# Performance work log

Hardware: AMD Instinct MI355X
Metric: run time of the kernel (lower is better)

## Reference

```python
import jax, jax.numpy as jnp
import numpy as np

K = 9          # kernel_size
PAD = K // 2   # 'same' padding, stride 1
SIGMA = 1.0
EPS = 1e-5     # BatchNorm eps

def _windows(a):
    # a: (B, C, L) -> (B, C, K, L); zero-padded sliding windows (== F.unfold semantics)
    L = a.shape[-1]
    ap = jnp.pad(a, ((0, 0), (0, 0), (PAD, PAD)))
    return jnp.stack([ap[:, :, k:k + L] for k in range(K)], axis=2)

def setup_inputs() -> dict:
    key = jax.random.key(0)
    ks = jax.random.split(key, 4)
    B, Cin, Cout, L = 8, 256, 256, 16384
    x = jax.random.normal(ks[0], (B, Cin, L), jnp.float32)
    coords = jax.random.uniform(ks[1], (B, 3, L), jnp.float32)
    conv_w = jax.random.normal(ks[2], (Cout, Cin, K), jnp.float32) * np.float32(1.0 / np.sqrt(Cin * K))
    conv_b = jnp.zeros((Cout,), jnp.float32)
    gamma = jnp.ones((Cout,), jnp.float32)
    beta = jnp.zeros((Cout,), jnp.float32)
    return {"x": x, "coords": coords, "conv_w": conv_w, "conv_b": conv_b, "gamma": gamma, "beta": beta}

def reference(x, coords, conv_w, conv_b, gamma, beta):
    # --- WeightedConv1D: Gaussian coordinate weights on each unfolded window element ---
    cw = _windows(coords)                                      # (B, 3, K, L)
    d2 = jnp.sum((cw - coords[:, :, None, :]) ** 2, axis=1)    # (B, K, L) squared dist to window center
    w = jnp.exp(-d2 / (2.0 * SIGMA ** 2))                      # (B, K, L) Gaussian weights
    xw = _windows(x) * w[:, None, :, :]                        # (B, Cin, K, L) weighted windows
    y = jnp.einsum('bckl,ock->bol', xw, conv_w) + conv_b[None, :, None]  # (B, Cout, L)
    # --- BatchNorm1d (training-mode batch statistics, biased variance) + ReLU ---
    mu = jnp.mean(y, axis=(0, 2), keepdims=True)
    var = jnp.var(y, axis=(0, 2), keepdims=True)
    yhat = (y - mu) * jax.lax.rsqrt(var + EPS)
    out = jax.nn.relu(yhat * gamma[None, :, None] + beta[None, :, None])
    # Dropout with drop=0.0 is the identity.
    return out
```

## Files before the change

kernel.cpp:

```cpp
#include <hip/hip_runtime.h>
#include <hip/hip_bf16.h>


typedef float        f32x4  __attribute__((ext_vector_type(4)));
typedef float        f32x16 __attribute__((ext_vector_type(16)));
typedef short        bf16x8 __attribute__((ext_vector_type(8)));
typedef unsigned int u32x4  __attribute__((ext_vector_type(4)));

#define LLEN 16384

__device__ __forceinline__ unsigned short bf16bits(float a) {
  return __builtin_bit_cast(unsigned short, __float2bfloat16(a));
}
__device__ __forceinline__ unsigned cvt_pk_bf16(float lo, float hi) {
  unsigned r;
  asm("v_cvt_pk_bf16_f32 %0, %1, %2" : "=v"(r) : "v"(lo), "v"(hi));
  return r;
}
__device__ __forceinline__ void gload16(const void* g, void* l) {
  __builtin_amdgcn_global_load_lds(
      (const __attribute__((address_space(1))) unsigned int*)g,
      (__attribute__((address_space(3))) unsigned int*)l, 16, 0, 0);
}

__global__ void k_prep(const float* __restrict__ cw,
                       unsigned short* __restrict__ A_r4,
                       unsigned short* __restrict__ A_gl,
                       float* __restrict__ sums, int big) {
  const int idx = blockIdx.x * 256 + threadIdx.x;
  if (idx < 1024) sums[idx] = 0.0f;
  const int o   = idx / 2304;
  const int rem = idx - o * 2304;
  const int c   = rem / 9;
  const int kk  = rem - c * 9;
  const unsigned short bits = bf16bits(cw[idx]);
  A_r4[((size_t)kk * 256 + o) * 256 + c] = bits;
  if (big) {
    const int cc = c >> 6, c6 = c & 63;
    const int u = (c6 >> 3) ^ (o & 7);
    A_gl[(size_t)((kk * 4 + cc) << 14) + ((o * 8 + u) << 3) + (c6 & 7)] = bits;
  }
}

__global__ void k_w(const float* __restrict__ coords, float* __restrict__ wbuf) {
  const int gidx = blockIdx.x * 256 + threadIdx.x;
  const int b = gidx >> 14, l = gidx & (LLEN - 1);
  const float* cb = coords + (size_t)b * 3 * LLEN;
  const float c0 = cb[l], c1 = cb[LLEN + l], c2v = cb[2 * LLEN + l];
#pragma unroll
  for (int kk = 0; kk < 9; ++kk) {
    const int lc = l + kk - 4;
    float a0 = 0.f, a1 = 0.f, a2 = 0.f;
    if (lc >= 0 && lc < LLEN) { a0 = cb[lc]; a1 = cb[LLEN + lc]; a2 = cb[2 * LLEN + lc]; }
    const float d0 = a0 - c0, d1 = a1 - c1, d2 = a2 - c2v;
    wbuf[(((size_t)(b * 9 + kk)) << 14) + l] = __expf(-0.5f * (d0 * d0 + d1 * d1 + d2 * d2));
  }
}

__global__ void k_xT(const float* __restrict__ x, unsigned short* __restrict__ xT) {
  __shared__ unsigned short T[64][72];
  const int tid = threadIdx.x, bid = blockIdx.x;
  const int ct = bid & 3, lt = (bid >> 2) & 255, b = bid >> 10;
  const int l0 = lt << 6, c0 = ct << 6;
#pragma unroll
  for (int p = 0; p < 4; ++p) {
    const int cl = p * 16 + (tid >> 4), ll = (tid & 15) << 2;
    const f32x4 v = *reinterpret_cast<const f32x4*>(
        x + (((size_t)(b * 256 + c0 + cl)) << 14) + l0 + ll);
#pragma unroll
    for (int q = 0; q < 4; ++q) T[cl][ll + q] = bf16bits(v[q]);
  }
  __syncthreads();
#pragma unroll
  for (int pass = 0; pass < 2; ++pass) {
    const int n = tid + pass * 256;
    const int ll = n >> 3, u = n & 7;
    const int l = l0 + ll;
    const int gsl = (u ^ (l & 7)) << 3;
    u32x4 val;
#pragma unroll
    for (int q = 0; q < 4; ++q)
      val[q] = (unsigned)T[gsl + 2 * q][ll] | ((unsigned)T[gsl + 2 * q + 1][ll] << 16);
    *reinterpret_cast<u32x4*>(xT + (((size_t)((b << 14) + l)) << 8) + (ct << 6) + (u << 3)) = val;
  }
}

__global__ __launch_bounds__(512, 2) void k_gemm_dma(
    const unsigned short* __restrict__ xT, const float* __restrict__ wbuf,
    const unsigned short* __restrict__ Agl, const float* __restrict__ convb,
    const unsigned short* __restrict__ zeros, float* __restrict__ y,
    float* __restrict__ sums) {
  __shared__ __align__(16) unsigned short Ash[2][16384];
  __shared__ __align__(16) unsigned short Xsh[2][17408];

  const int tid = threadIdx.x, lane = tid & 63, wv = tid >> 6;
  const int wm = wv >> 2, wn = wv & 3;
  const int l31 = lane & 31, hi5 = lane >> 5;
  const int b = blockIdx.x >> 6, lt = blockIdx.x & 63, l0 = lt << 8;

  f32x16 acc[4][2];
#pragma unroll
  for (int i = 0; i < 4; ++i)
#pragma unroll
    for (int j = 0; j < 2; ++j) acc[i][j] = (f32x16)(0.0f);

  auto dmaA = [&](int ab, int kk, int cc) {
#pragma unroll
    for (int call = 0; call < 4; ++call) {
      const int n0 = ((call << 3) + wv) << 6;
      gload16(Agl + (((size_t)((kk << 2) + cc)) << 14) + (((size_t)(n0 + lane)) << 3),
              (char*)&Ash[ab][0] + n0 * 16);
    }
  };
  auto dmaX = [&](int xb, int ncc, int slot) {
    const int id = (slot << 3) + wv;
    if (id < 34) {
      const int n0 = id << 6;
      const int n = n0 + lane;
      const int r = n >> 3, u = n & 7;
      const int lp = l0 - 4 + r;
      const unsigned short* src =
          (lp >= 0 && lp < LLEN)
              ? xT + (((size_t)((b << 14) + lp)) << 8) + (ncc << 6) + (u << 3)
              : zeros;
      gload16(src, (char*)&Xsh[xb][0] + n0 * 16);
    }
  };

  dmaA(0, 0, 0);
#pragma unroll
  for (int s = 0; s < 5; ++s) dmaX(0, 0, s);
  float wl[2], wt[2];
#pragma unroll
  for (int nt = 0; nt < 2; ++nt)
    wl[nt] = wbuf[((size_t)(b * 9) << 14) + l0 + wn * 64 + nt * 32 + l31];
  __syncthreads();

  int ab = 0;
#pragma unroll 1
  for (int cc = 0; cc < 4; ++cc) {
    const int xb = cc & 1;
    const char* XshB = (const char*)&Xsh[xb][0];
#pragma unroll 1
    for (int kk = 0; kk < 9; ++kk) {
      const bool last = (cc == 3) && (kk == 8);
      const int nkk = (kk == 8) ? 0 : kk + 1;
      const int ncc = (kk == 8) ? cc + 1 : cc;
      if (!last) {
        dmaA(ab ^ 1, nkk, ncc);
#pragma unroll
        for (int nt = 0; nt < 2; ++nt)
          wt[nt] = wbuf[((size_t)(b * 9 + nkk) << 14) + l0 + wn * 64 + nt * 32 + l31];
      }
      if (cc < 3 && kk < 5) dmaX(xb ^ 1, cc + 1, kk);

      const char* AshB = (const char*)&Ash[ab][0];
#pragma unroll
      for (int ks = 0; ks < 4; ++ks) {
        const int g = (ks << 1) + hi5;
        bf16x8 bfr[2];
#pragma unroll
        for (int nt = 0; nt < 2; ++nt) {
          const int rr = wn * 64 + nt * 32 + l31 + kk;
          const u32x4 xv = *reinterpret_cast<const u32x4*>(
              XshB + rr * 128 + ((g ^ ((rr + 4) & 7)) << 4));
          u32x4 o4;
#pragma unroll
          for (int q = 0; q < 4; ++q) {
            const float flo = __builtin_bit_cast(float, xv[q] << 16) * wl[nt];
            const float fhi = __builtin_bit_cast(float, xv[q] & 0xffff0000u) * wl[nt];
            o4[q] = cvt_pk_bf16(flo, fhi);
          }
          bfr[nt] = __builtin_bit_cast(bf16x8, o4);
        }
#pragma unroll
        for (int mt = 0; mt < 4; ++mt) {
          const int o = wm * 128 + mt * 32 + l31;
          const bf16x8 af = *reinterpret_cast<const bf16x8*>(
              AshB + o * 128 + ((g ^ (l31 & 7)) << 4));
#pragma unroll
          for (int nt = 0; nt < 2; ++nt)
            acc[mt][nt] = __builtin_amdgcn_mfma_f32_32x32x16_bf16(af, bfr[nt],
                                                                  acc[mt][nt], 0, 0, 0);
        }
      }
      __syncthreads();
      ab ^= 1;
      wl[0] = wt[0]; wl[1] = wt[1];
    }
  }

  float* red = reinterpret_cast<float*>(&Xsh[0][0]);
  red[tid] = 0.0f;
  __syncthreads();
#pragma unroll
  for (int mt = 0; mt < 4; ++mt) {
#pragma unroll
    for (int v = 0; v < 16; ++v) {
      const int o = wm * 128 + mt * 32 + (v & 3) + 8 * (v >> 2) + 4 * hi5;
      const float cb = convb[o];
      float s = 0.f, s2 = 0.f;
#pragma unroll
      for (int nt = 0; nt < 2; ++nt) {
        const int l = l0 + wn * 64 + nt * 32 + l31;
        const float yv = acc[mt][nt][v] + cb;
        y[(((size_t)b * 256 + o) << 14) + l] = yv;
        s += yv; s2 += yv * yv;
      }
#pragma unroll
      for (int d = 1; d < 32; d <<= 1) { s += __shfl_xor(s, d); s2 += __shfl_xor(s2, d); }
      if (l31 == 0) { atomicAdd(&red[o], s); atomicAdd(&red[o + 256], s2); }
    }
  }
  __syncthreads();
  atomicAdd(&sums[tid], red[tid]);
}

__global__ __launch_bounds__(512, 2) void k_gemm_fb(
    const float* __restrict__ x, const float* __restrict__ wbuf,
    const unsigned short* __restrict__ Aperm, const float* __restrict__ convb,
    float* __restrict__ y, float* __restrict__ sums) {
  __shared__ __align__(16) unsigned short Ash[2][256 * 64];
  __shared__ __align__(16) unsigned short Xsh[2][264 * 72];

  const int tid  = threadIdx.x;
  const int lane = tid & 63, wv = tid >> 6;
  const int wm = wv >> 2, wn = wv & 3;
  const int hi = lane >> 4, lo16 = lane & 15;
  const int b  = blockIdx.x >> 6, lt = blockIdx.x & 63;
  const int l0 = lt << 8;
  const int nbase = wn * 64 + lo16;
  const int c = tid >> 3, rg = tid & 7;

  f32x4 acc[8][4];
#pragma unroll
  for (int i = 0; i < 8; ++i)
#pragma unroll
    for (int j = 0; j < 4; ++j) acc[i][j] = f32x4{0.f, 0.f, 0.f, 0.f};

  auto loadA = [&](int kk, int cc, u32x4 (&dst)[4]) {
#pragma unroll
    for (int p = 0; p < 4; ++p) {
      const int row = p * 64 + (tid >> 3);
      dst[p] = *reinterpret_cast<const u32x4*>(
          Aperm + ((size_t)kk * 256 + row) * 256 + cc * 64 + ((tid & 7) << 3));
    }
  };
  auto writeA = [&](int ab, const u32x4 (&src)[4]) {
#pragma unroll
    for (int p = 0; p < 4; ++p) {
      const int row  = p * 64 + (tid >> 3);
      const unsigned byte = (unsigned)(row * 128 + (((tid & 7) ^ (row & 7)) << 4));
      *reinterpret_cast<u32x4*>(reinterpret_cast<char*>(&Ash[ab][0]) + byte) = src[p];
    }
  };
  auto loadPiece = [&](int ncc, int i) -> f32x4 {
    const float* xrow = x + ((size_t)(b * 256 + ncc * 64 + c)) * LLEN;
    const int grp = rg + 8 * i;
    const int lx = l0 - 4 + grp * 4;
    f32x4 v = {0.f, 0.f, 0.f, 0.f};
    if (grp < 66 && lx >= 0 && lx <= LLEN - 4)
      v = *reinterpret_cast<const f32x4*>(xrow + lx);
    return v;
  };
  auto writePiece = [&](int xb, int i, const f32x4& v) {
    const int grp = rg + 8 * i;
    if (grp < 66) {
      unsigned short* base = &Xsh[xb][0] + (grp * 4) * 72 + c;
      base[0]   = bf16bits(v[0]);
      base[72]  = bf16bits(v[1]);
      base[144] = bf16bits(v[2]);
      base[216] = bf16bits(v[3]);
    }
  };

  {
    u32x4 a0[4];
    loadA(0, 0, a0);
    writeA(0, a0);
#pragma unroll
    for (int i = 0; i < 9; ++i) writePiece(0, i, loadPiece(0, i));
  }
  float wl[4];
#pragma unroll
  for (int nt = 0; nt < 4; ++nt)
    wl[nt] = wbuf[((size_t)(b * 9) << 14) + l0 + nbase + nt * 16];
  __syncthreads();

  int ab = 0;
  f32x4 xhold = {0.f, 0.f, 0.f, 0.f};

#pragma unroll 1
  for (int cc = 0; cc < 4; ++cc) {
    const int xb = cc & 1;
#pragma unroll 1
    for (int kk = 0; kk < 9; ++kk) {
      const int nkk = (kk == 8) ? 0 : kk + 1;
      const int ncc = (kk == 8) ? cc + 1 : cc;
      const bool has_next = (ncc < 4);

      u32x4 areg[4];
      if (has_next) loadA(nkk, ncc, areg);
      float wln[4] = {0.f, 0.f, 0.f, 0.f};
      if (has_next) {
#pragma unroll
        for (int nt = 0; nt < 4; ++nt)
          wln[nt] = wbuf[((size_t)(b * 9 + nkk) << 14) + l0 + nbase + nt * 16];
      }
      f32x4 xnew = {0.f, 0.f, 0.f, 0.f};
      if (cc < 3) xnew = loadPiece(cc + 1, kk);

      const char* AshB = reinterpret_cast<const char*>(&Ash[ab][0]);
      const char* XshB = reinterpret_cast<const char*>(&Xsh[xb][0]);
#pragma unroll
      for (int kb = 0; kb < 2; ++kb) {
        bf16x8 bfr[4];
#pragma unroll
        for (int nt = 0; nt < 4; ++nt) {
          const int r = nbase + nt * 16 + kk;
          const u32x4 xv = *reinterpret_cast<const u32x4*>(XshB + r * 144 + kb * 64 + hi * 16);
          const float wv2 = wl[nt];
          u32x4 o4;
#pragma unroll
          for (int q = 0; q < 4; ++q) {
            const float flo = __builtin_bit_cast(float, xv[q] << 16) * wv2;
            const float fhi = __builtin_bit_cast(float, xv[q] & 0xffff0000u) * wv2;
            o4[q] = cvt_pk_bf16(flo, fhi);
          }
          bfr[nt] = __builtin_bit_cast(bf16x8, o4);
        }
#pragma unroll
        for (int mt = 0; mt < 8; ++mt) {
          const int orow = wm * 128 + mt * 16 + lo16;
          const unsigned aoff = (unsigned)(orow * 128 + (((kb * 4 + hi) ^ (orow & 7)) << 4));
          const bf16x8 af = *reinterpret_cast<const bf16x8*>(AshB + aoff);
#pragma unroll
          for (int nt = 0; nt < 4; ++nt)
            acc[mt][nt] = __builtin_amdgcn_mfma_f32_16x16x32_bf16(af, bfr[nt],
                                                                  acc[mt][nt], 0, 0, 0);
        }
      }

      if (cc < 3 && kk >= 1) writePiece(xb ^ 1, kk - 1, xhold);
      if (cc < 3 && kk == 8) writePiece(xb ^ 1, 8, xnew);
      if (has_next) writeA(ab ^ 1, areg);

      __syncthreads();
      ab ^= 1;
      xhold = xnew;
#pragma unroll
      for (int nt = 0; nt < 4; ++nt) wl[nt] = wln[nt];
    }
  }

  float* red = reinterpret_cast<float*>(&Ash[0][0]);
  red[tid] = 0.0f;
  __syncthreads();
#pragma unroll
  for (int mt = 0; mt < 8; ++mt) {
#pragma unroll
    for (int v = 0; v < 4; ++v) {
      const int o = wm * 128 + mt * 16 + hi * 4 + v;
      const float cb = convb[o];
      float s = 0.f, s2 = 0.f;
#pragma unroll
      for (int nt = 0; nt < 4; ++nt) {
        const int l = l0 + nbase + nt * 16;
        const float yv = acc[mt][nt][v] + cb;
        y[(((size_t)b * 256 + o) << 14) + l] = yv;
        s += yv; s2 += yv * yv;
      }
#pragma unroll
      for (int d = 1; d < 16; d <<= 1) { s += __shfl_xor(s, d); s2 += __shfl_xor(s2, d); }
      if (lo16 == 0) { atomicAdd(&red[o], s); atomicAdd(&red[o + 256], s2); }
    }
  }
  __syncthreads();
  atomicAdd(&sums[tid], red[tid]);
}

__global__ void k_norm(float* __restrict__ y, const float* __restrict__ sums,
                       const float* __restrict__ gamma, const float* __restrict__ beta) {
  const size_t i0 = ((size_t)blockIdx.x * 256 + threadIdx.x) * 8;
  const int o = (int)((i0 >> 14) & 255);
  const float n = 131072.f;
  const float mu = sums[o] / n;
  float var = sums[256 + o] / n - mu * mu;
  var = fmaxf(var, 0.f);
  const float sc = rsqrtf(var + 1e-5f) * gamma[o];
  const float bb = beta[o] - mu * sc;
  f32x4 v0 = *reinterpret_cast<const f32x4*>(y + i0);
  f32x4 v1 = *reinterpret_cast<const f32x4*>(y + i0 + 4);
#pragma unroll
  for (int i = 0; i < 4; ++i) {
    v0[i] = fmaxf(v0[i] * sc + bb, 0.f);
    v1[i] = fmaxf(v1[i] * sc + bb, 0.f);
  }
  *reinterpret_cast<f32x4*>(y + i0) = v0;
  *reinterpret_cast<f32x4*>(y + i0 + 4) = v1;
}

extern "C" void kernel_launch(void* const* d_in, const int* in_sizes, int n_in,
                              void* d_out, int out_size, void* d_ws, size_t ws_size,
                              hipStream_t stream) {
  const float* x      = (const float*)d_in[0];
  const float* coords = (const float*)d_in[1];
  const float* conv_w = (const float*)d_in[2];
  const float* conv_b = (const float*)d_in[3];
  const float* gamma  = (const float*)d_in[4];
  const float* beta   = (const float*)d_in[5];
  float* out = (float*)d_out;

  float* sums = (float*)d_ws;
  const unsigned short* zeros = (const unsigned short*)((char*)d_ws + 2048);
  float* wbuf = (float*)((char*)d_ws + 4096);
  unsigned short* A_r4 = (unsigned short*)((char*)d_ws + 4096 + (size_t)8 * 9 * LLEN * 4);
  unsigned short* A_gl = A_r4 + 589824;
  unsigned short* xT   = A_gl + 589824;
  const size_t need = 4096 + (size_t)8 * 9 * LLEN * 4 + 2 * 1179648ull + 67108864ull;
  const int big = (ws_size >= need) ? 1 : 0;

  k_prep<<<2304, 256, 0, stream>>>(conv_w, A_r4, A_gl, sums, big);
  k_w<<<512, 256, 0, stream>>>(coords, wbuf);
  if (big) {
    k_xT<<<8192, 256, 0, stream>>>(x, xT);
    k_gemm_dma<<<512, 512, 0, stream>>>(xT, wbuf, A_gl, conv_b, zeros, out, sums);
  } else {
    k_gemm_fb<<<512, 512, 0, stream>>>(x, wbuf, A_r4, conv_b, out, sums);
  }
  k_norm<<<16384, 256, 0, stream>>>(out, sums, gamma, beta);
}
```

Baseline: 287.5 us.

## Pre-weight X tiles once in LDS per tap and store intermediate y as bf16

The GEMM kernel now loads x rows into registers, multiplies them by the Gaussian weight once per tap and stores weighted bf16 tiles into double-buffered LDS. This replaces the per-MFMA-fragment reweighting and the direct global-to-LDS DMA of X. A-fragment loads are grouped ahead of the MFMAs and wrapped in s_setprio. When enough workspace is available, the pre-norm y is written as bf16 rather than fp32, which halves that intermediate write and the norm kernel's read but adds rounding error before BatchNorm.

```diff
diff --git a/kernel.cpp b/kernel.cpp
--- a/kernel.cpp
+++ b/kernel.cpp
@@ -21,6 +21,12 @@
   __builtin_amdgcn_global_load_lds(
       (const __attribute__((address_space(1))) unsigned int*)g,
       (__attribute__((address_space(3))) unsigned int*)l, 16, 0, 0);
+}
+__device__ __forceinline__ float bflo(unsigned u) {
+  return __builtin_bit_cast(float, u << 16);
+}
+__device__ __forceinline__ float bfhi(unsigned u) {
+  return __builtin_bit_cast(float, u & 0xffff0000u);
 }
 
 __global__ void k_prep(const float* __restrict__ cw,
@@ -85,18 +91,20 @@
   }
 }
 
-__global__ __launch_bounds__(512, 2) void k_gemm_dma(
+template <int YBF>
+__global__ __launch_bounds__(512, 2) void k_gemm_w(
     const unsigned short* __restrict__ xT, const float* __restrict__ wbuf,
     const unsigned short* __restrict__ Agl, const float* __restrict__ convb,
-    const unsigned short* __restrict__ zeros, float* __restrict__ y,
+    float* __restrict__ yf, unsigned short* __restrict__ ybf,
     float* __restrict__ sums) {
   __shared__ __align__(16) unsigned short Ash[2][16384];
-  __shared__ __align__(16) unsigned short Xsh[2][17408];
+  __shared__ __align__(16) unsigned short Xw[2][264 * 64];
 
   const int tid = threadIdx.x, lane = tid & 63, wv = tid >> 6;
   const int wm = wv >> 2, wn = wv & 3;
   const int l31 = lane & 31, hi5 = lane >> 5;
   const int b = blockIdx.x >> 6, lt = blockIdx.x & 63, l0 = lt << 8;
+  const int rbase = tid >> 3, uu = tid & 7;
 
   f32x16 acc[4][2];
 #pragma unroll
@@ -112,85 +120,97 @@
               (char*)&Ash[ab][0] + n0 * 16);
     }
   };
-  auto dmaX = [&](int xb, int ncc, int slot) {
-    const int id = (slot << 3) + wv;
-    if (id < 34) {
-      const int n0 = id << 6;
-      const int n = n0 + lane;
-      const int r = n >> 3, u = n & 7;
-      const int lp = l0 - 4 + r;
-      const unsigned short* src =
-          (lp >= 0 && lp < LLEN)
-              ? xT + (((size_t)((b << 14) + lp)) << 8) + (ncc << 6) + (u << 3)
-              : zeros;
-      gload16(src, (char*)&Xsh[xb][0] + n0 * 16);
-    }
-  };
-
+  auto loadX = [&](int cc, int i) -> u32x4 {
+    u32x4 v = {0u, 0u, 0u, 0u};
+    if (i < 4 || tid < 64) {
+      const int r = rbase + 64 * i;
+      const int l = l0 - 4 + r;
+      if (l >= 0 && l < LLEN)
+        v = *reinterpret_cast<const u32x4*>(
+            xT + (((size_t)((b << 14) + l)) << 8) + cc * 64 + uu * 8);
+    }
+    return v;
+  };
+  auto stage = [&](int xwb, int nkk, const u32x4 (&xr)[5]) {
+    const float* wrow = wbuf + ((size_t)(b * 9 + nkk) << 14);
+#pragma unroll
+    for (int i = 0; i < 5; ++i) {
+      if (i < 4 || tid < 64) {
+        const int r = rbase + 64 * i;
+        int lo_ = l0 + r - nkk;
+        lo_ = lo_ < 0 ? 0 : (lo_ > LLEN - 1 ? LLEN - 1 : lo_);
+        const float wv2 = wrow[lo_];
+        u32x4 o4;
+#pragma unroll
+        for (int q = 0; q < 4; ++q)
+          o4[q] = cvt_pk_bf16(bflo(xr[i][q]) * wv2, bfhi(xr[i][q]) * wv2);
+        *reinterpret_cast<u32x4*>(
+            reinterpret_cast<char*>(&Xw[xwb][0]) + r * 128 + ((uu ^ 4) << 4)) = o4;
+      }
+    }
+  };
+
+  u32x4 xcur[5], xnext[5];
+#pragma unroll
+  for (int i = 0; i < 5; ++i) xcur[i] = loadX(0, i);
   dmaA(0, 0, 0);
-#pragma unroll
-  for (int s = 0; s < 5; ++s) dmaX(0, 0, s);
-  float wl[2], wt[2];
-#pragma unroll
-  for (int nt = 0; nt < 2; ++nt)
-    wl[nt] = wbuf[((size_t)(b * 9) << 14) + l0 + wn * 64 + nt * 32 + l31];
-  __syncthreads();
-
-  int ab = 0;
+  stage(0, 0, xcur);
+  __syncthreads();
+
+  int ab = 0, xwb = 0;
 #pragma unroll 1
   for (int cc = 0; cc < 4; ++cc) {
-    const int xb = cc & 1;
-    const char* XshB = (const char*)&Xsh[xb][0];
 #pragma unroll 1
     for (int kk = 0; kk < 9; ++kk) {
       const bool last = (cc == 3) && (kk == 8);
       const int nkk = (kk == 8) ? 0 : kk + 1;
       const int ncc = (kk == 8) ? cc + 1 : cc;
-      if (!last) {
-        dmaA(ab ^ 1, nkk, ncc);
-#pragma unroll
-        for (int nt = 0; nt < 2; ++nt)
-          wt[nt] = wbuf[((size_t)(b * 9 + nkk) << 14) + l0 + wn * 64 + nt * 32 + l31];
-      }
-      if (cc < 3 && kk < 5) dmaX(xb ^ 1, cc + 1, kk);
+      if (!last) dmaA(ab ^ 1, nkk, ncc);
+      if (cc < 3 && kk >= 4) xnext[kk - 4] = loadX(cc + 1, kk - 4);
 
       const char* AshB = (const char*)&Ash[ab][0];
+      const char* XwB  = (const char*)&Xw[xwb][0];
 #pragma unroll
       for (int ks = 0; ks < 4; ++ks) {
         const int g = (ks << 1) + hi5;
         bf16x8 bfr[2];
 #pragma unroll
         for (int nt = 0; nt < 2; ++nt) {
-          const int rr = wn * 64 + nt * 32 + l31 + kk;
-          const u32x4 xv = *reinterpret_cast<const u32x4*>(
-              XshB + rr * 128 + ((g ^ ((rr + 4) & 7)) << 4));
-          u32x4 o4;
-#pragma unroll
-          for (int q = 0; q < 4; ++q) {
-            const float flo = __builtin_bit_cast(float, xv[q] << 16) * wl[nt];
-            const float fhi = __builtin_bit_cast(float, xv[q] & 0xffff0000u) * wl[nt];
-            o4[q] = cvt_pk_bf16(flo, fhi);
-          }
-          bfr[nt] = __builtin_bit_cast(bf16x8, o4);
+          const int R = wn * 64 + nt * 32 + l31 + kk;
+          bfr[nt] = *reinterpret_cast<const bf16x8*>(
+              XwB + R * 128 + ((g ^ (R & 7)) << 4));
         }
+        bf16x8 afr[4];
 #pragma unroll
         for (int mt = 0; mt < 4; ++mt) {
           const int o = wm * 128 + mt * 32 + l31;
-          const bf16x8 af = *reinterpret_cast<const bf16x8*>(
+          afr[mt] = *reinterpret_cast<const bf16x8*>(
               AshB + o * 128 + ((g ^ (l31 & 7)) << 4));
+        }
+        __builtin_amdgcn_s_setprio(1);
+#pragma unroll
+        for (int mt = 0; mt < 4; ++mt)
 #pragma unroll
           for (int nt = 0; nt < 2; ++nt)
-            acc[mt][nt] = __builtin_amdgcn_mfma_f32_32x32x16_bf16(af, bfr[nt],
+            acc[mt][nt] = __builtin_amdgcn_mfma_f32_32x32x16_bf16(afr[mt], bfr[nt],
                                                                   acc[mt][nt], 0, 0, 0);
-        }
+        __builtin_amdgcn_s_setprio(0);
+      }
+
+      if (!last) {
+        if (kk < 8) stage(xwb ^ 1, nkk, xcur);
+        else        stage(xwb ^ 1, 0, xnext);
       }
       __syncthreads();
-      ab ^= 1;
-      wl[0] = wt[0]; wl[1] = wt[1];
-    }
-  }
-
-  float* red = reinterpret_cast<float*>(&Xsh[0][0]);
+      ab ^= 1; xwb ^= 1;
+    }
+    if (cc < 3) {
+#pragma unroll
+      for (int i = 0; i < 5; ++i) xcur[i] = xnext[i];
+    }
+  }
+
+  float* red = reinterpret_cast<float*>(&Xw[0][0]);
   red[tid] = 0.0f;
   __syncthreads();
 #pragma unroll
@@ -204,7 +224,9 @@
       for (int nt = 0; nt < 2; ++nt) {
         const int l = l0 + wn * 64 + nt * 32 + l31;
         const float yv = acc[mt][nt][v] + cb;
-        y[(((size_t)b * 256 + o) << 14) + l] = yv;
+        const size_t idx = (((size_t)b * 256 + o) << 14) + l;
+        if (YBF) ybf[idx] = bf16bits(yv);
+        else     yf[idx] = yv;
         s += yv; s2 += yv * yv;
       }
 #pragma unroll
@@ -322,11 +344,8 @@
           const float wv2 = wl[nt];
           u32x4 o4;
 #pragma unroll
-          for (int q = 0; q < 4; ++q) {
-            const float flo = __builtin_bit_cast(float, xv[q] << 16) * wv2;
-            const float fhi = __builtin_bit_cast(float, xv[q] & 0xffff0000u) * wv2;
-            o4[q] = cvt_pk_bf16(flo, fhi);
-          }
+          for (int q = 0; q < 4; ++q)
+            o4[q] = cvt_pk_bf16(bflo(xv[q]) * wv2, bfhi(xv[q]) * wv2);
           bfr[nt] = __builtin_bit_cast(bf16x8, o4);
         }
 #pragma unroll
@@ -379,7 +398,9 @@
   atomicAdd(&sums[tid], red[tid]);
 }
 
-__global__ void k_norm(float* __restrict__ y, const float* __restrict__ sums,
+template <int YBF>
+__global__ void k_norm(const float* __restrict__ yf, const unsigned short* __restrict__ ybf,
+                       float* __restrict__ out, const float* __restrict__ sums,
                        const float* __restrict__ gamma, const float* __restrict__ beta) {
   const size_t i0 = ((size_t)blockIdx.x * 256 + threadIdx.x) * 8;
   const int o = (int)((i0 >> 14) & 255);
@@ -389,15 +410,27 @@
   var = fmaxf(var, 0.f);
   const float sc = rsqrtf(var + 1e-5f) * gamma[o];
   const float bb = beta[o] - mu * sc;
-  f32x4 v0 = *reinterpret_cast<const f32x4*>(y + i0);
-  f32x4 v1 = *reinterpret_cast<const f32x4*>(y + i0 + 4);
+  f32x4 v0, v1;
+  if (YBF) {
+    const u32x4 u = *reinterpret_cast<const u32x4*>(ybf + i0);
+#pragma unroll
+    for (int i = 0; i < 4; ++i) {
+      const unsigned w = u[i];
+      float a = bflo(w), c = bfhi(w);
+      if (i < 2) { v0[2 * i] = a; v0[2 * i + 1] = c; }
+      else       { v1[2 * (i - 2)] = a; v1[2 * (i - 2) + 1] = c; }
+    }
+  } else {
+    v0 = *reinterpret_cast<const f32x4*>(yf + i0);
+    v1 = *reinterpret_cast<const f32x4*>(yf + i0 + 4);
+  }
 #pragma unroll
   for (int i = 0; i < 4; ++i) {
     v0[i] = fmaxf(v0[i] * sc + bb, 0.f);
     v1[i] = fmaxf(v1[i] * sc + bb, 0.f);
   }
-  *reinterpret_cast<f32x4*>(y + i0) = v0;
-  *reinterpret_cast<f32x4*>(y + i0 + 4) = v1;
+  *reinterpret_cast<f32x4*>(out + i0) = v0;
+  *reinterpret_cast<f32x4*>(out + i0 + 4) = v1;
 }
 
 extern "C" void kernel_launch(void* const* d_in, const int* in_sizes, int n_in,
@@ -412,21 +445,29 @@
   float* out = (float*)d_out;
 
   float* sums = (float*)d_ws;
-  const unsigned short* zeros = (const unsigned short*)((char*)d_ws + 2048);
   float* wbuf = (float*)((char*)d_ws + 4096);
   unsigned short* A_r4 = (unsigned short*)((char*)d_ws + 4096 + (size_t)8 * 9 * LLEN * 4);
   unsigned short* A_gl = A_r4 + 589824;
   unsigned short* xT   = A_gl + 589824;
-  const size_t need = 4096 + (size_t)8 * 9 * LLEN * 4 + 2 * 1179648ull + 67108864ull;
-  const int big = (ws_size >= need) ? 1 : 0;
+  unsigned short* ybf  = xT + 33554432;
+  const size_t need_big = 4096 + (size_t)8 * 9 * LLEN * 4 + 2 * 1179648ull + 67108864ull;
+  const size_t need_ybf = need_big + 67108864ull;
+  const int big  = (ws_size >= need_big) ? 1 : 0;
+  const int ybfp = (ws_size >= need_ybf) ? 1 : 0;
 
   k_prep<<<2304, 256, 0, stream>>>(conv_w, A_r4, A_gl, sums, big);
   k_w<<<512, 256, 0, stream>>>(coords, wbuf);
   if (big) {
     k_xT<<<8192, 256, 0, stream>>>(x, xT);
-    k_gemm_dma<<<512, 512, 0, stream>>>(xT, wbuf, A_gl, conv_b, zeros, out, sums);
+    if (ybfp) {
+      k_gemm_w<1><<<512, 512, 0, stream>>>(xT, wbuf, A_gl, conv_b, out, ybf, sums);
+      k_norm<1><<<16384, 256, 0, stream>>>(out, ybf, out, sums, gamma, beta);
+    } else {
+      k_gemm_w<0><<<512, 512, 0, stream>>>(xT, wbuf, A_gl, conv_b, out, ybf, sums);
+      k_norm<0><<<16384, 256, 0, stream>>>(out, ybf, out, sums, gamma, beta);
+    }
   } else {
     k_gemm_fb<<<512, 512, 0, stream>>>(x, wbuf, A_r4, conv_b, out, sums);
-  }
-  k_norm<<<16384, 256, 0, stream>>>(out, sums, gamma, beta);
-}
+    k_norm<0><<<16384, 256, 0, stream>>>(out, nullptr, out, sums, gamma, beta);
+  }
+}
```

Result: slower. 316.8 us (+10.2%).

## Switch GEMM to 16x16 MFMA tiles and stage pre-norm output in bf16

Applied to the files above, without the earlier changes.

Rewrites the main GEMM kernel to use 16x16x32 bf16 MFMA with an 8x4 accumulator tile per wave. It also issues LDS reads for the next k-half before the current MFMAs, to overlap loads with compute. When workspace allows, the pre-BatchNorm output is stored as bf16 in a scratch buffer instead of fp32 into the output. This halves that intermediate write and the norm kernel's read, and trims duplicate weight-layout writes in prep. The cost is extra rounding of y before normalization, and a different register footprint.

```diff
diff --git a/kernel.cpp b/kernel.cpp
--- a/kernel.cpp
+++ b/kernel.cpp
@@ -3,7 +3,6 @@
 
 
 typedef float        f32x4  __attribute__((ext_vector_type(4)));
-typedef float        f32x16 __attribute__((ext_vector_type(16)));
 typedef short        bf16x8 __attribute__((ext_vector_type(8)));
 typedef unsigned int u32x4  __attribute__((ext_vector_type(4)));
 
@@ -22,10 +21,15 @@
       (const __attribute__((address_space(1))) unsigned int*)g,
       (__attribute__((address_space(3))) unsigned int*)l, 16, 0, 0);
 }
+__device__ __forceinline__ float bflo(unsigned u) {
+  return __builtin_bit_cast(float, u << 16);
+}
+__device__ __forceinline__ float bfhi(unsigned u) {
+  return __builtin_bit_cast(float, u & 0xffff0000u);
+}
 
 __global__ void k_prep(const float* __restrict__ cw,
-                       unsigned short* __restrict__ A_r4,
-                       unsigned short* __restrict__ A_gl,
+                       unsigned short* __restrict__ AU,
                        float* __restrict__ sums, int big) {
   const int idx = blockIdx.x * 256 + threadIdx.x;
   if (idx < 1024) sums[idx] = 0.0f;
@@ -34,11 +38,12 @@
   const int c   = rem / 9;
   const int kk  = rem - c * 9;
   const unsigned short bits = bf16bits(cw[idx]);
-  A_r4[((size_t)kk * 256 + o) * 256 + c] = bits;
   if (big) {
     const int cc = c >> 6, c6 = c & 63;
     const int u = (c6 >> 3) ^ (o & 7);
-    A_gl[(size_t)((kk * 4 + cc) << 14) + ((o * 8 + u) << 3) + (c6 & 7)] = bits;
+    AU[(size_t)((kk * 4 + cc) << 14) + ((o * 8 + u) << 3) + (c6 & 7)] = bits;
+  } else {
+    AU[((size_t)kk * 256 + o) * 256 + c] = bits;
   }
 }
 
@@ -85,24 +90,26 @@
   }
 }
 
-__global__ __launch_bounds__(512, 2) void k_gemm_dma(
+template <int YBF>
+__global__ __launch_bounds__(512, 2) void k_gemm16(
     const unsigned short* __restrict__ xT, const float* __restrict__ wbuf,
     const unsigned short* __restrict__ Agl, const float* __restrict__ convb,
-    const unsigned short* __restrict__ zeros, float* __restrict__ y,
-    float* __restrict__ sums) {
+    const unsigned short* __restrict__ zeros, float* __restrict__ yf,
+    unsigned short* __restrict__ ybf, float* __restrict__ sums) {
   __shared__ __align__(16) unsigned short Ash[2][16384];
   __shared__ __align__(16) unsigned short Xsh[2][17408];
 
   const int tid = threadIdx.x, lane = tid & 63, wv = tid >> 6;
   const int wm = wv >> 2, wn = wv & 3;
-  const int l31 = lane & 31, hi5 = lane >> 5;
+  const int hi = lane >> 4, lo16 = lane & 15;
   const int b = blockIdx.x >> 6, lt = blockIdx.x & 63, l0 = lt << 8;
-
-  f32x16 acc[4][2];
-#pragma unroll
-  for (int i = 0; i < 4; ++i)
-#pragma unroll
-    for (int j = 0; j < 2; ++j) acc[i][j] = (f32x16)(0.0f);
+  const int nbase = wn * 64 + lo16;
+
+  f32x4 acc[8][4];
+#pragma unroll
+  for (int i = 0; i < 8; ++i)
+#pragma unroll
+    for (int j = 0; j < 4; ++j) acc[i][j] = f32x4{0.f, 0.f, 0.f, 0.f};
 
   auto dmaA = [&](int ab, int kk, int cc) {
 #pragma unroll
@@ -130,10 +137,10 @@
   dmaA(0, 0, 0);
 #pragma unroll
   for (int s = 0; s < 5; ++s) dmaX(0, 0, s);
-  float wl[2], wt[2];
-#pragma unroll
-  for (int nt = 0; nt < 2; ++nt)
-    wl[nt] = wbuf[((size_t)(b * 9) << 14) + l0 + wn * 64 + nt * 32 + l31];
+  float wl[4], wt[4];
+#pragma unroll
+  for (int nt = 0; nt < 4; ++nt)
+    wl[nt] = wbuf[((size_t)(b * 9) << 14) + l0 + nbase + nt * 16];
   __syncthreads();
 
   int ab = 0;
@@ -149,44 +156,75 @@
       if (!last) {
         dmaA(ab ^ 1, nkk, ncc);
 #pragma unroll
-        for (int nt = 0; nt < 2; ++nt)
-          wt[nt] = wbuf[((size_t)(b * 9 + nkk) << 14) + l0 + wn * 64 + nt * 32 + l31];
+        for (int nt = 0; nt < 4; ++nt)
+          wt[nt] = wbuf[((size_t)(b * 9 + nkk) << 14) + l0 + nbase + nt * 16];
       }
       if (cc < 3 && kk < 5) dmaX(xb ^ 1, cc + 1, kk);
 
       const char* AshB = (const char*)&Ash[ab][0];
-#pragma unroll
-      for (int ks = 0; ks < 4; ++ks) {
-        const int g = (ks << 1) + hi5;
-        bf16x8 bfr[2];
-#pragma unroll
-        for (int nt = 0; nt < 2; ++nt) {
-          const int rr = wn * 64 + nt * 32 + l31 + kk;
-          const u32x4 xv = *reinterpret_cast<const u32x4*>(
-              XshB + rr * 128 + ((g ^ ((rr + 4) & 7)) << 4));
-          u32x4 o4;
-#pragma unroll
-          for (int q = 0; q < 4; ++q) {
-            const float flo = __builtin_bit_cast(float, xv[q] << 16) * wl[nt];
-            const float fhi = __builtin_bit_cast(float, xv[q] & 0xffff0000u) * wl[nt];
-            o4[q] = cvt_pk_bf16(flo, fhi);
-          }
-          bfr[nt] = __builtin_bit_cast(bf16x8, o4);
-        }
-#pragma unroll
-        for (int mt = 0; mt < 4; ++mt) {
-          const int o = wm * 128 + mt * 32 + l31;
-          const bf16x8 af = *reinterpret_cast<const bf16x8*>(
-              AshB + o * 128 + ((g ^ (l31 & 7)) << 4));
-#pragma unroll
-          for (int nt = 0; nt < 2; ++nt)
-            acc[mt][nt] = __builtin_amdgcn_mfma_f32_32x32x16_bf16(af, bfr[nt],
-                                                                  acc[mt][nt], 0, 0, 0);
-        }
-      }
+      u32x4 xv0[4];
+#pragma unroll
+      for (int nt = 0; nt < 4; ++nt) {
+        const int rr = nbase + nt * 16 + kk;
+        xv0[nt] = *reinterpret_cast<const u32x4*>(
+            XshB + rr * 128 + ((hi ^ ((rr + 4) & 7)) << 4));
+      }
+      bf16x8 a0[8];
+#pragma unroll
+      for (int mt = 0; mt < 8; ++mt) {
+        const int o = wm * 128 + mt * 16 + lo16;
+        a0[mt] = *reinterpret_cast<const bf16x8*>(
+            AshB + o * 128 + ((hi ^ (lo16 & 7)) << 4));
+      }
+      bf16x8 b0[4];
+#pragma unroll
+      for (int nt = 0; nt < 4; ++nt) {
+        u32x4 o4;
+#pragma unroll
+        for (int q = 0; q < 4; ++q)
+          o4[q] = cvt_pk_bf16(bflo(xv0[nt][q]) * wl[nt], bfhi(xv0[nt][q]) * wl[nt]);
+        b0[nt] = __builtin_bit_cast(bf16x8, o4);
+      }
+      u32x4 xv1[4];
+#pragma unroll
+      for (int nt = 0; nt < 4; ++nt) {
+        const int rr = nbase + nt * 16 + kk;
+        xv1[nt] = *reinterpret_cast<const u32x4*>(
+            XshB + rr * 128 + (((4 + hi) ^ ((rr + 4) & 7)) << 4));
+      }
+#pragma unroll
+      for (int mt = 0; mt < 8; ++mt)
+#pragma unroll
+        for (int nt = 0; nt < 4; ++nt)
+          acc[mt][nt] = __builtin_amdgcn_mfma_f32_16x16x32_bf16(a0[mt], b0[nt],
+                                                                acc[mt][nt], 0, 0, 0);
+      bf16x8 a1[8];
+#pragma unroll
+      for (int mt = 0; mt < 8; ++mt) {
+        const int o = wm * 128 + mt * 16 + lo16;
+        a1[mt] = *reinterpret_cast<const bf16x8*>(
+            AshB + o * 128 + (((4 + hi) ^ (lo16 & 7)) << 4));
+      }
+      bf16x8 b1[4];
+#pragma unroll
+      for (int nt = 0; nt < 4; ++nt) {
+        u32x4 o4;
+#pragma unroll
+        for (int q = 0; q < 4; ++q)
+          o4[q] = cvt_pk_bf16(bflo(xv1[nt][q]) * wl[nt], bfhi(xv1[nt][q]) * wl[nt]);
+        b1[nt] = __builtin_bit_cast(bf16x8, o4);
+      }
+#pragma unroll
+      for (int mt = 0; mt < 8; ++mt)
+#pragma unroll
+        for (int nt = 0; nt < 4; ++nt)
+          acc[mt][nt] = __builtin_amdgcn_mfma_f32_16x16x32_bf16(a1[mt], b1[nt],
+                                                                acc[mt][nt], 0, 0, 0);
+
       __syncthreads();
       ab ^= 1;
-      wl[0] = wt[0]; wl[1] = wt[1];
+#pragma unroll
+      for (int nt = 0; nt < 4; ++nt) wl[nt] = wt[nt];
     }
   }
 
@@ -194,22 +232,24 @@
   red[tid] = 0.0f;
   __syncthreads();
 #pragma unroll
-  for (int mt = 0; mt < 4; ++mt) {
-#pragma unroll
-    for (int v = 0; v < 16; ++v) {
-      const int o = wm * 128 + mt * 32 + (v & 3) + 8 * (v >> 2) + 4 * hi5;
+  for (int mt = 0; mt < 8; ++mt) {
+#pragma unroll
+    for (int v = 0; v < 4; ++v) {
+      const int o = wm * 128 + mt * 16 + hi * 4 + v;
       const float cb = convb[o];
       float s = 0.f, s2 = 0.f;
 #pragma unroll
-      for (int nt = 0; nt < 2; ++nt) {
-        const int l = l0 + wn * 64 + nt * 32 + l31;
+      for (int nt = 0; nt < 4; ++nt) {
+        const int l = l0 + nbase + nt * 16;
         const float yv = acc[mt][nt][v] + cb;
-        y[(((size_t)b * 256 + o) << 14) + l] = yv;
+        const size_t idx = (((size_t)b * 256 + o) << 14) + l;
+        if (YBF) ybf[idx] = bf16bits(yv);
+        else     yf[idx] = yv;
         s += yv; s2 += yv * yv;
       }
 #pragma unroll
-      for (int d = 1; d < 32; d <<= 1) { s += __shfl_xor(s, d); s2 += __shfl_xor(s2, d); }
-      if (l31 == 0) { atomicAdd(&red[o], s); atomicAdd(&red[o + 256], s2); }
+      for (int d = 1; d < 16; d <<= 1) { s += __shfl_xor(s, d); s2 += __shfl_xor(s2, d); }
+      if (lo16 == 0) { atomicAdd(&red[o], s); atomicAdd(&red[o + 256], s2); }
     }
   }
   __syncthreads();
@@ -319,14 +359,10 @@
         for (int nt = 0; nt < 4; ++nt) {
           const int r = nbase + nt * 16 + kk;
           const u32x4 xv = *reinterpret_cast<const u32x4*>(XshB + r * 144 + kb * 64 + hi * 16);
-          const float wv2 = wl[nt];
           u32x4 o4;
 #pragma unroll
-          for (int q = 0; q < 4; ++q) {
-            const float flo = __builtin_bit_cast(float, xv[q] << 16) * wv2;
-            const float fhi = __builtin_bit_cast(float, xv[q] & 0xffff0000u) * wv2;
-            o4[q] = cvt_pk_bf16(flo, fhi);
-          }
+          for (int q = 0; q < 4; ++q)
+            o4[q] = cvt_pk_bf16(bflo(xv[q]) * wl[nt], bfhi(xv[q]) * wl[nt]);
           bfr[nt] = __builtin_bit_cast(bf16x8, o4);
         }
 #pragma unroll
@@ -379,7 +415,9 @@
   atomicAdd(&sums[tid], red[tid]);
 }
 
-__global__ void k_norm(float* __restrict__ y, const float* __restrict__ sums,
+template <int YBF>
+__global__ void k_norm(const float* __restrict__ yf, const unsigned short* __restrict__ ybf,
+                       float* __restrict__ out, const float* __restrict__ sums,
                        const float* __restrict__ gamma, const float* __restrict__ beta) {
   const size_t i0 = ((size_t)blockIdx.x * 256 + threadIdx.x) * 8;
   const int o = (int)((i0 >> 14) & 255);
@@ -389,15 +427,27 @@
   var = fmaxf(var, 0.f);
   const float sc = rsqrtf(var + 1e-5f) * gamma[o];
   const float bb = beta[o] - mu * sc;
-  f32x4 v0 = *reinterpret_cast<const f32x4*>(y + i0);
-  f32x4 v1 = *reinterpret_cast<const f32x4*>(y + i0 + 4);
+  f32x4 v0, v1;
+  if (YBF) {
+    const u32x4 u = *reinterpret_cast<const u32x4*>(ybf + i0);
+#pragma unroll
+    for (int i = 0; i < 4; ++i) {
+      const unsigned w = u[i];
+      float a = bflo(w), c = bfhi(w);
+      if (i < 2) { v0[2 * i] = a; v0[2 * i + 1] = c; }
+      else       { v1[2 * (i - 2)] = a; v1[2 * (i - 2) + 1] = c; }
+    }
+  } else {
+    v0 = *reinterpret_cast<const f32x4*>(yf + i0);
+    v1 = *reinterpret_cast<const f32x4*>(yf + i0 + 4);
+  }
 #pragma unroll
   for (int i = 0; i < 4; ++i) {
     v0[i] = fmaxf(v0[i] * sc + bb, 0.f);
     v1[i] = fmaxf(v1[i] * sc + bb, 0.f);
   }
-  *reinterpret_cast<f32x4*>(y + i0) = v0;
-  *reinterpret_cast<f32x4*>(y + i0 + 4) = v1;
+  *reinterpret_cast<f32x4*>(out + i0) = v0;
+  *reinterpret_cast<f32x4*>(out + i0 + 4) = v1;
 }
 
 extern "C" void kernel_launch(void* const* d_in, const int* in_sizes, int n_in,
@@ -414,19 +464,27 @@
   float* sums = (float*)d_ws;
   const unsigned short* zeros = (const unsigned short*)((char*)d_ws + 2048);
   float* wbuf = (float*)((char*)d_ws + 4096);
-  unsigned short* A_r4 = (unsigned short*)((char*)d_ws + 4096 + (size_t)8 * 9 * LLEN * 4);
-  unsigned short* A_gl = A_r4 + 589824;
-  unsigned short* xT   = A_gl + 589824;
-  const size_t need = 4096 + (size_t)8 * 9 * LLEN * 4 + 2 * 1179648ull + 67108864ull;
-  const int big = (ws_size >= need) ? 1 : 0;
-
-  k_prep<<<2304, 256, 0, stream>>>(conv_w, A_r4, A_gl, sums, big);
+  unsigned short* AU  = (unsigned short*)((char*)d_ws + 4096 + (size_t)8 * 9 * LLEN * 4);
+  unsigned short* xT  = AU + 589824;
+  unsigned short* ybf = xT + 33554432;
+  const size_t need_big = 4096 + (size_t)8 * 9 * LLEN * 4 + 1179648ull + 67108864ull;
+  const size_t need_ybf = need_big + 67108864ull;
+  const int big  = (ws_size >= need_big) ? 1 : 0;
+  const int ybfp = (ws_size >= need_ybf) ? 1 : 0;
+
+  k_prep<<<2304, 256, 0, stream>>>(conv_w, AU, sums, big);
   k_w<<<512, 256, 0, stream>>>(coords, wbuf);
   if (big) {
     k_xT<<<8192, 256, 0, stream>>>(x, xT);
-    k_gemm_dma<<<512, 512, 0, stream>>>(xT, wbuf, A_gl, conv_b, zeros, out, sums);
+    if (ybfp) {
+      k_gemm16<1><<<512, 512, 0, stream>>>(xT, wbuf, AU, conv_b, zeros, out, ybf, sums);
+      k_norm<1><<<16384, 256, 0, stream>>>(out, ybf, out, sums, gamma, beta);
+    } else {
+      k_gemm16<0><<<512, 512, 0, stream>>>(xT, wbuf, AU, conv_b, zeros, out, ybf, sums);
+      k_norm<0><<<16384, 256, 0, stream>>>(out, ybf, out, sums, gamma, beta);
+    }
   } else {
-    k_gemm_fb<<<512, 512, 0, stream>>>(x, wbuf, A_r4, conv_b, out, sums);
-  }
-  k_norm<<<16384, 256, 0, stream>>>(out, sums, gamma, beta);
-}
+    k_gemm_fb<<<512, 512, 0, stream>>>(x, wbuf, AU, conv_b, out, sums);
+    k_norm<0><<<16384, 256, 0, stream>>>(out, (const unsigned short*)out, out, sums, gamma, beta);
+  }
+}
```

Result: faster. 254.4 us (-11.5%).
